# Kernel optimization log

Hardware: AMD Instinct MI355X
Metric: run time of the kernel (lower is better)

Reference implementation:

```python
import jax, jax.numpy as jnp
import numpy as np

B, S, D, H = 2, 2048, 1024, 16
DK = D // H


def setup_inputs() -> dict:
    key = jax.random.key(0)
    ks = jax.random.split(key, 8)
    s = 1.0 / np.sqrt(D)
    return {
        "query": jax.random.normal(ks[0], (B, S, D), jnp.float32),
        "key": jax.random.normal(ks[1], (B, S, D), jnp.float32),
        "value": jax.random.normal(ks[2], (B, S, D), jnp.float32),
        "mask": jnp.ones((B, S), jnp.int32),
        "w_q": jax.random.normal(ks[3], (D, D), jnp.float32) * s,
        "w_k": jax.random.normal(ks[4], (D, D), jnp.float32) * s,
        "w_v": jax.random.normal(ks[5], (D, D), jnp.float32) * s,
        "w_o": jax.random.normal(ks[6], (D, D), jnp.float32) * s,
        "b_o": jnp.zeros((D,), jnp.float32),
    }


def reference(query, key, value, mask, w_q, w_k, w_v, w_o, b_o):
    scale = np.sqrt(DK).astype(np.float32)
    # Linear layers: torch stores weight as [out, in], y = x @ W.T
    Q = (query @ w_q.T).reshape(B, S, H, DK).transpose(0, 2, 1, 3)  # [B,H,S,DK]
    K = (key @ w_k.T).reshape(B, S, H, DK).transpose(0, 2, 1, 3)
    V = (value @ w_v.T).reshape(B, S, H, DK).transpose(0, 2, 1, 3)
    scores = jnp.einsum("bhqd,bhkd->bhqk", Q, K) / scale  # [B,H,S,S]
    m = mask[:, None, None, :]  # [B,1,1,S]
    scores = jnp.where(m == 0, jnp.float32(-1e9), scores)
    attn = jax.nn.softmax(scores, axis=-1)  # dropout in eval mode = identity
    ctx = jnp.einsum("bhqk,bhkd->bhqd", attn, V)
    ctx = ctx.transpose(0, 2, 1, 3).reshape(B, S, D)
    out = ctx @ w_o.T + b_o
    return out, attn
```

## Files before the change

### kernel.cpp

```cpp
#include <hip/hip_runtime.h>
#include <hip/hip_bf16.h>
#include <math.h>

#define B 2
#define S 2048
#define D 1024
#define H 16
#define DK 64

typedef __attribute__((ext_vector_type(8))) short bf8;
typedef __attribute__((ext_vector_type(8))) unsigned short u16x8;
typedef __attribute__((ext_vector_type(4))) unsigned short u16x4;
typedef __attribute__((ext_vector_type(4))) float f32x4;
typedef unsigned short ush;

__device__ __forceinline__ float bf2f(ush u) {
    union { unsigned int i; float f; } v; v.i = ((unsigned int)u) << 16; return v.f;
}
__device__ __forceinline__ ush f2bf_rne(float x) {
    __hip_bfloat16 h = __float2bfloat16(x);
    union { __hip_bfloat16 h; ush u; } v; v.h = h; return v.u;
}
__device__ __forceinline__ ush f2bf_trunc(float x) {
    union { float f; unsigned int i; } v; v.f = x; return (ush)(v.i >> 16);
}

__device__ __forceinline__ void gl16(const void* g, void* l) {
    __builtin_amdgcn_global_load_lds(
        (const __attribute__((address_space(1))) void*)g,
        (__attribute__((address_space(3))) void*)l, 16, 0, 0);
}

#define FENCE()    asm volatile("" ::: "memory")
#define WAIT_VM(N) asm volatile("s_waitcnt vmcnt(" #N ")" ::: "memory")
#define BARRAW()   __builtin_amdgcn_s_barrier()

__global__ __launch_bounds__(256) void conv_tri_k(
    const float* __restrict__ A, ush* __restrict__ Ah, ush* __restrict__ Al, int nbA,
    const float* __restrict__ Bsrc, ush* __restrict__ Bh, ush* __restrict__ Bl, int nbB,
    const float* __restrict__ C, ush* __restrict__ Ch)
{
    const int bx = blockIdx.x;
    const float* src; ush* oh; ush* ol; size_t t;
    if (bx < nbA)            { src = A;    oh = Ah; ol = Al;      t = (size_t)bx * 256 + threadIdx.x; }
    else if (bx < nbA + nbB) { src = Bsrc; oh = Bh; ol = Bl;      t = (size_t)(bx - nbA) * 256 + threadIdx.x; }
    else                     { src = C;    oh = Ch; ol = nullptr; t = (size_t)(bx - nbA - nbB) * 256 + threadIdx.x; }

    const float4* s4 = (const float4*)src + t * 2;
    float4 a = s4[0], c = s4[1];
    float v[8] = {a.x, a.y, a.z, a.w, c.x, c.y, c.z, c.w};
    u16x8 hi;
#pragma unroll
    for (int j = 0; j < 8; ++j) hi[j] = f2bf_trunc(v[j]);
    *(u16x8*)&oh[t * 8] = hi;
    if (ol) {
        u16x8 lo;
#pragma unroll
        for (int j = 0; j < 8; ++j) lo[j] = f2bf_rne(v[j] - bf2f(hi[j]));
        *(u16x8*)&ol[t * 8] = lo;
    }
}

template<bool SPLIT, int EPI>
__global__ __launch_bounds__(512) void gemm_bf3(
    const ush* __restrict__ Xh, const ush* __restrict__ Xl,
    const ush* __restrict__ Wh, const ush* __restrict__ Wl,
    const float* __restrict__ bias, void* __restrict__ Y0v, void* __restrict__ Y1v)
{
    const int tid  = threadIdx.x;
    const int lane = tid & 63;
    const int w    = tid >> 6;
    const int wn   = w >> 2;
    const int wm   = w & 3;
    const int m0   = blockIdx.x * 128;
    const int n0   = blockIdx.y * 128;

    __shared__ __align__(16) ush BufS[4][256 * 64];

    f32x4 acc[4][2];
#pragma unroll
    for (int s = 0; s < 4; ++s)
#pragma unroll
        for (int t = 0; t < 2; ++t) acc[s][t] = (f32x4){0.f, 0.f, 0.f, 0.f};

    const int kg = (lane >> 4) * 8;
    const int rb = lane >> 3;
    const int jd = lane & 7;
    const int kS = SPLIT ? 32 : 16;

    auto stage = [&](ush* buf, int ks) {
#pragma unroll
        for (int i = 0; i < 4; ++i) {
            int rd = w * 32 + i * 8 + rb;
            int jo = jd ^ (rd & 7);
            const ush* src;
            if (rd < 128) {
                if (SPLIT)
                    src = (jo < 4) ? Xh + (size_t)(n0 + rd) * 1024 + ks * 32 + jo * 8
                                   : Xl + (size_t)(n0 + rd) * 1024 + ks * 32 + (jo - 4) * 8;
                else
                    src = Xh + (size_t)(n0 + rd) * 1024 + ks * 64 + jo * 8;
            } else {
                int rw = rd - 128;
                if (SPLIT)
                    src = (jo < 4) ? Wh + (size_t)(m0 + rw) * 1024 + ks * 32 + jo * 8
                                   : Wl + (size_t)(m0 + rw) * 1024 + ks * 32 + (jo - 4) * 8;
                else
                    src = Wh + (size_t)(m0 + rw) * 1024 + ks * 64 + jo * 8;
            }
            gl16(src, &buf[(w * 32 + i * 8) * 64]);
        }
    };

    auto step = [&](const ush* buf) {
        bf8 a0[4], a1[4], b0[2], b1[2];
#pragma unroll
        for (int s = 0; s < 4; ++s) {
            int r = wn * 64 + s * 16 + (lane & 15);
            a0[s] = *(const bf8*)&buf[r * 64 + (kg ^ ((r & 7) << 3))];
            a1[s] = *(const bf8*)&buf[r * 64 + ((32 + kg) ^ ((r & 7) << 3))];
        }
#pragma unroll
        for (int t = 0; t < 2; ++t) {
            int r = wm * 32 + t * 16 + (lane & 15);
            b0[t] = *(const bf8*)&buf[(128 + r) * 64 + (kg ^ ((r & 7) << 3))];
            b1[t] = *(const bf8*)&buf[(128 + r) * 64 + ((32 + kg) ^ ((r & 7) << 3))];
        }
#pragma unroll
        for (int s = 0; s < 4; ++s)
#pragma unroll
            for (int t = 0; t < 2; ++t) {
                acc[s][t] = __builtin_amdgcn_mfma_f32_16x16x32_bf16(a0[s], b0[t], acc[s][t], 0, 0, 0);
                if (SPLIT) {
                    acc[s][t] = __builtin_amdgcn_mfma_f32_16x16x32_bf16(a0[s], b1[t], acc[s][t], 0, 0, 0);
                    acc[s][t] = __builtin_amdgcn_mfma_f32_16x16x32_bf16(a1[s], b0[t], acc[s][t], 0, 0, 0);
                } else {
                    acc[s][t] = __builtin_amdgcn_mfma_f32_16x16x32_bf16(a1[s], b1[t], acc[s][t], 0, 0, 0);
                }
            }
    };

    stage(&BufS[0][0], 0);
    stage(&BufS[1][0], 1);
    stage(&BufS[2][0], 2);
    FENCE();
    WAIT_VM(8); BARRAW(); FENCE();

    for (int kt = 0; kt < kS; ++kt) {
        const int pf = kt + 3;
        if (pf < kS) { stage(&BufS[pf & 3][0], pf); FENCE(); }
        step(&BufS[kt & 3][0]);
        if (kt + 3 < kS)      { WAIT_VM(8); }
        else if (kt + 2 < kS) { WAIT_VM(4); }
        else if (kt + 1 < kS) { WAIT_VM(0); }
        BARRAW(); FENCE();
    }

#pragma unroll
    for (int s = 0; s < 4; ++s)
#pragma unroll
        for (int t = 0; t < 2; ++t) {
            const int nb = n0 + wn * 64 + 16 * s + 4 * (lane >> 4);
            const int m  = m0 + wm * 32 + 16 * t + (lane & 15);
            if (EPI == 0) {
                float* Y = (float*)Y0v;
                const float bb = bias[m];
#pragma unroll
                for (int r = 0; r < 4; ++r)
                    Y[(size_t)(nb + r) * 1024 + m] = acc[s][t][r] + bb;
            } else if (EPI == 1) {
                ush* Yh = (ush*)Y0v;
                ush* Yl = (ush*)Y1v;
#pragma unroll
                for (int r = 0; r < 4; ++r) {
                    float v = acc[s][t][r];
                    ush hi = f2bf_trunc(v);
                    Yh[(size_t)(nb + r) * 1024 + m] = hi;
                    Yl[(size_t)(nb + r) * 1024 + m] = f2bf_rne(v - bf2f(hi));
                }
            } else {
                ush* Vt = (ush*)Y0v;
                u16x4 pk;
#pragma unroll
                for (int r = 0; r < 4; ++r) pk[r] = f2bf_rne(acc[s][t][r]);
                size_t addr = ((size_t)(nb >> 11) * 1024 + m) * 2048 + (nb & 2047);
                *(u16x4*)&Vt[addr] = pk;
            }
        }
}

__global__ __launch_bounds__(512) void attn_mfma4(
    const ush* __restrict__ Qh, const ush* __restrict__ Ql,
    const ush* __restrict__ Kh, const ush* __restrict__ Kl,
    const ush* __restrict__ Vt, const int* __restrict__ maskg,
    float* __restrict__ attn, ush* __restrict__ ctx)
{
    const int tid  = threadIdx.x;
    const int lane = tid & 63;
    const int w    = tid >> 6;
    const int lid  = blockIdx.x + (blockIdx.y << 4) + (blockIdx.z << 8);
    const int swz  = ((lid & 7) << 6) | (lid >> 3);
    const int qt = swz & 15, h = (swz >> 4) & 15, b = swz >> 8;
    const int q0 = qt * 128;

    __shared__ __align__(16) ush KhsD[3][4096];
    __shared__ __align__(16) ush KlsD[2][4096];
    __shared__ __align__(16) ush VtsD[2][4096];
    __shared__ __align__(16) ush Pus[8][1024];
    __shared__ float biasS[2048];

    const int kg = (lane >> 4) * 8;
    const int q  = lane & 15;
    const int qrow = q0 + w * 16 + q;
    const int rb = lane >> 3;
    const int jd = lane & 7;

    const ush* KhT = Kh + (size_t)(b * S) * 1024 + h * DK;
    const ush* KlT = Kl + (size_t)(b * S) * 1024 + h * DK;
    const ush* VtT = Vt + (size_t)(b * 1024 + h * DK) * 2048;

    {
        const int t4 = tid * 4;
        int4 mv = *(const int4*)&maskg[b * S + t4];
        biasS[t4 + 0] = mv.x ? 0.f : -1e9f;
        biasS[t4 + 1] = mv.y ? 0.f : -1e9f;
        biasS[t4 + 2] = mv.z ? 0.f : -1e9f;
        biasS[t4 + 3] = mv.w ? 0.f : -1e9f;
    }

    bf8 qh[2], ql[2];
    {
        const ush* p1 = Qh + (size_t)(b * S + qrow) * D + h * DK + kg;
        qh[0] = *(const bf8*)p1; qh[1] = *(const bf8*)(p1 + 32);
        const ush* p2 = Ql + (size_t)(b * S + qrow) * D + h * DK + kg;
        ql[0] = *(const bf8*)p2; ql[1] = *(const bf8*)(p2 + 32);
    }

    const int rd = w * 8 + rb;
    const int jo = jd ^ (rd & 7);

    auto stKh = [&](int bufi, int k0) {
        gl16(KhT + (size_t)(k0 + rd) * 1024 + jo * 8, &KhsD[bufi][(w * 8) * 64]);
    };
    auto stKl = [&](int bufi, int k0) {
        gl16(KlT + (size_t)(k0 + rd) * 1024 + jo * 8, &KlsD[bufi][(w * 8) * 64]);
    };
    auto stVt = [&](int bufi, int k0) {
        gl16(VtT + (size_t)rd * 2048 + k0 + jo * 8, &VtsD[bufi][(w * 8) * 64]);
    };

    const float scale = 0.125f;
    float mrow = -1e30f, lrow = 0.f;

    auto computeA = [&](const ush* Khs_, int k0) {
        f32x4 sacc[4];
#pragma unroll
        for (int st = 0; st < 4; ++st) sacc[st] = (f32x4){0.f, 0.f, 0.f, 0.f};
#pragma unroll
        for (int st = 0; st < 4; ++st) {
            int r = st * 16 + q;
#pragma unroll
            for (int dh = 0; dh < 2; ++dh) {
                bf8 kf = *(const bf8*)&Khs_[r * 64 + ((dh * 32 + kg) ^ ((r & 7) << 3))];
                sacc[st] = __builtin_amdgcn_mfma_f32_16x16x32_bf16(kf, qh[dh], sacc[st], 0, 0, 0);
            }
        }
        f32x4 bias_r[4];
#pragma unroll
        for (int st = 0; st < 4; ++st)
            bias_r[st] = *(const f32x4*)&biasS[k0 + st * 16 + (lane >> 4) * 4];
        float tmax = -1e30f;
#pragma unroll
        for (int st = 0; st < 4; ++st)
#pragma unroll
            for (int rr = 0; rr < 4; ++rr)
                tmax = fmaxf(tmax, sacc[st][rr] * scale + bias_r[st][rr]);
        tmax = fmaxf(tmax, __shfl_xor(tmax, 16));
        tmax = fmaxf(tmax, __shfl_xor(tmax, 32));
        const float nm = fmaxf(mrow, tmax);
        float ts = 0.f;
#pragma unroll
        for (int st = 0; st < 4; ++st)
#pragma unroll
            for (int rr = 0; rr < 4; ++rr)
                ts += __expf(sacc[st][rr] * scale + bias_r[st][rr] - nm);
        ts += __shfl_xor(ts, 16);
        ts += __shfl_xor(ts, 32);
        lrow = lrow * __expf(mrow - nm) + ts;
        mrow = nm;
    };

    stKh(0, 0); stKh(1, 64);
    __syncthreads();
    {
        int cur = 0, nxt = 2;
        for (int kt = 0; kt < 32; ++kt) {
            if (kt + 2 < 32) stKh(nxt, (kt + 2) * 64);
            FENCE();
            computeA(&KhsD[cur][0], kt * 64);
            if (kt < 30) { WAIT_VM(1); } else { WAIT_VM(0); }
            BARRAW(); FENCE();
            cur = (cur == 2) ? 0 : cur + 1;
            nxt = (nxt == 2) ? 0 : nxt + 1;
        }
    }
    const float inv_l = 1.f / lrow;

    f32x4 cacc[4];
#pragma unroll
    for (int dt = 0; dt < 4; ++dt) cacc[dt] = (f32x4){0.f, 0.f, 0.f, 0.f};
    float* attn_bh = attn + (size_t)(b * H + h) * S * S;

    auto computeB = [&](int bsel, int k0) {
        const ush* Khs_ = &KhsD[bsel][0];
        const ush* Kls_ = &KlsD[bsel][0];
        const ush* Vts_ = &VtsD[bsel][0];
        f32x4 sacc[4];
#pragma unroll
        for (int st = 0; st < 4; ++st) sacc[st] = (f32x4){0.f, 0.f, 0.f, 0.f};
#pragma unroll
        for (int st = 0; st < 4; ++st) {
            int r = st * 16 + q;
#pragma unroll
            for (int dh = 0; dh < 2; ++dh) {
                bf8 kf = *(const bf8*)&Khs_[r * 64 + ((dh * 32 + kg) ^ ((r & 7) << 3))];
                bf8 lf = *(const bf8*)&Kls_[r * 64 + ((dh * 32 + kg) ^ ((r & 7) << 3))];
                sacc[st] = __builtin_amdgcn_mfma_f32_16x16x32_bf16(kf, qh[dh], sacc[st], 0, 0, 0);
                sacc[st] = __builtin_amdgcn_mfma_f32_16x16x32_bf16(kf, ql[dh], sacc[st], 0, 0, 0);
                sacc[st] = __builtin_amdgcn_mfma_f32_16x16x32_bf16(lf, qh[dh], sacc[st], 0, 0, 0);
            }
        }
#pragma unroll
        for (int st = 0; st < 4; ++st) {
            f32x4 bias_r = *(const f32x4*)&biasS[k0 + st * 16 + (lane >> 4) * 4];
            float pv[4];
#pragma unroll
            for (int rr = 0; rr < 4; ++rr)
                pv[rr] = __expf(sacc[st][rr] * scale + bias_r[rr] - mrow) * inv_l;
            float4 f4 = {pv[0], pv[1], pv[2], pv[3]};
            *(float4*)&attn_bh[(size_t)(q0 + w * 16 + q) * S + k0 + st * 16 + (lane >> 4) * 4] = f4;
#pragma unroll
            for (int rp = 0; rp < 2; ++rp) {
                int key = st * 16 + (lane >> 4) * 4 + rp * 2;
                unsigned int pk = (unsigned int)f2bf_rne(pv[rp * 2]) |
                                  ((unsigned int)f2bf_rne(pv[rp * 2 + 1]) << 16);
                *(unsigned int*)&Pus[w][q * 64 + (key ^ ((q & 7) << 3))] = pk;
            }
        }
        bf8 pa[2];
        pa[0] = *(const bf8*)&Pus[w][q * 64 + ((kg)      ^ ((q & 7) << 3))];
        pa[1] = *(const bf8*)&Pus[w][q * 64 + ((32 + kg) ^ ((q & 7) << 3))];
#pragma unroll
        for (int dt = 0; dt < 4; ++dt) {
            int r = dt * 16 + q;
#pragma unroll
            for (int kc2 = 0; kc2 < 2; ++kc2) {
                bf8 vf = *(const bf8*)&Vts_[r * 64 + ((kc2 * 32 + kg) ^ ((r & 7) << 3))];
                cacc[dt] = __builtin_amdgcn_mfma_f32_16x16x32_bf16(pa[kc2], vf, cacc[dt], 0, 0, 0);
            }
        }
    };

    stKh(0, 0); stKl(0, 0); stVt(0, 0);
    FENCE();
    WAIT_VM(0); BARRAW(); FENCE();
    {
        int cur = 0;
        for (int kt = 0; kt < 32; ++kt) {
            if (kt + 1 < 32) {
                const int kN = (kt + 1) * 64;
                stKh(cur ^ 1, kN); stKl(cur ^ 1, kN); stVt(cur ^ 1, kN);
            }
            FENCE();
            computeB(cur, kt * 64);
            if (kt + 1 < 32) { WAIT_VM(4); } else { FENCE(); }
            BARRAW(); FENCE();
            cur ^= 1;
        }
    }

#pragma unroll
    for (int dt = 0; dt < 4; ++dt)
#pragma unroll
        for (int rr = 0; rr < 4; ++rr) {
            int qq = q0 + w * 16 + 4 * (lane >> 4) + rr;
            ctx[(size_t)(b * S + qq) * D + h * DK + dt * 16 + (lane & 15)] =
                f2bf_rne(cacc[dt][rr]);
        }
}

extern "C" void kernel_launch(void* const* d_in, const int* in_sizes, int n_in,
                              void* d_out, int out_size, void* d_ws, size_t ws_size,
                              hipStream_t stream)
{
    const float* query = (const float*)d_in[0];
    const float* key   = (const float*)d_in[1];
    const float* value = (const float*)d_in[2];
    const int*   mask  = (const int*)d_in[3];
    const float* w_q   = (const float*)d_in[4];
    const float* w_k   = (const float*)d_in[5];
    const float* w_v   = (const float*)d_in[6];
    const float* w_o   = (const float*)d_in[7];
    const float* b_o   = (const float*)d_in[8];

    float* out  = (float*)d_out;
    float* attn = out + (size_t)B * S * D;

    const size_t NE = (size_t)B * S * D;
    const size_t WE = (size_t)D * D;

    ush* Qh = (ush*)d_ws;
    ush* Ql = Qh + NE;
    ush* Kh = Ql + NE;
    ush* Kl = Kh + NE;
    ush* Vt = Kl + NE;
    ush* Cb = Vt + NE;

    ush* qXh = (ush*)attn;
    ush* qXl = qXh + NE;
    ush* kXh = qXl + NE;
    ush* kXl = kXh + NE;
    ush* vXh = kXl + NE;
    ush* wqH = vXh + NE;
    ush* wqL = wqH + WE;
    ush* wkH = wqL + WE;
    ush* wkL = wkH + WE;
    ush* wvH = wkL + WE;
    ush* woH = Qh;

    const dim3 blk(256);
    const dim3 gblk(512);
    const dim3 ggrid(D / 128, (B * S) / 128);
    const dim3 agrid(S / 128, H, B);

    const int nbX = (int)(NE / 8 / 256);
    const int nbW = (int)(WE / 8 / 256);

    conv_tri_k<<<dim3(nbX + nbW + nbX), blk, 0, stream>>>(
        query, qXh, qXl, nbX, w_q, wqH, wqL, nbW, value, vXh);
    conv_tri_k<<<dim3(nbX + nbW + nbW), blk, 0, stream>>>(
        key, kXh, kXl, nbX, w_k, wkH, wkL, nbW, w_v, wvH);

    gemm_bf3<true, 1><<<ggrid, gblk, 0, stream>>>(qXh, qXl, wqH, wqL, nullptr, Qh, Ql);
    gemm_bf3<true, 1><<<ggrid, gblk, 0, stream>>>(kXh, kXl, wkH, wkL, nullptr, Kh, Kl);
    gemm_bf3<false, 2><<<ggrid, gblk, 0, stream>>>(vXh, nullptr, wvH, nullptr, nullptr, Vt, nullptr);

    attn_mfma4<<<agrid, dim3(512), 0, stream>>>(Qh, Ql, Kh, Kl, Vt, mask, attn, Cb);

    conv_tri_k<<<dim3(nbW), blk, 0, stream>>>(
        nullptr, nullptr, nullptr, 0, nullptr, nullptr, nullptr, 0, w_o, woH);
    gemm_bf3<false, 0><<<ggrid, gblk, 0, stream>>>(Cb, nullptr, woH, nullptr, b_o, out, nullptr);
}
```

Baseline: 344.4 us.

## Merge conversion and QKV projection launches; use nontemporal stores for outputs

Folds the two input-conversion launches into one kernel that dispatches on block index, and folds the three Q/K/V projection GEMMs into one launch that picks the projection from blockIdx.z. The aim is fewer kernel launches and less tail idle time, since a single larger grid can fill the GPU while the three GEMMs run together. The attention-probability stores and the output GEMM stores now use nontemporal stores to avoid polluting the cache with large write-only data. The risk is heterogeneous work inside the merged GEMM grid (the V path does half the MFMA steps), which gives uneven block durations.

```diff
diff --git a/kernel.cpp b/kernel.cpp
--- a/kernel.cpp
+++ b/kernel.cpp
@@ -35,37 +35,64 @@
 #define WAIT_VM(N) asm volatile("s_waitcnt vmcnt(" #N ")" ::: "memory")
 #define BARRAW()   __builtin_amdgcn_s_barrier()
 
-__global__ __launch_bounds__(256) void conv_tri_k(
-    const float* __restrict__ A, ush* __restrict__ Ah, ush* __restrict__ Al, int nbA,
-    const float* __restrict__ Bsrc, ush* __restrict__ Bh, ush* __restrict__ Bl, int nbB,
-    const float* __restrict__ C, ush* __restrict__ Ch)
-{
-    const int bx = blockIdx.x;
-    const float* src; ush* oh; ush* ol; size_t t;
-    if (bx < nbA)            { src = A;    oh = Ah; ol = Al;      t = (size_t)bx * 256 + threadIdx.x; }
-    else if (bx < nbA + nbB) { src = Bsrc; oh = Bh; ol = Bl;      t = (size_t)(bx - nbA) * 256 + threadIdx.x; }
-    else                     { src = C;    oh = Ch; ol = nullptr; t = (size_t)(bx - nbA - nbB) * 256 + threadIdx.x; }
+__global__ __launch_bounds__(256) void conv_hex_k(
+    const float* __restrict__ q,  ush* __restrict__ qh,  ush* __restrict__ qlo,
+    const float* __restrict__ wq, ush* __restrict__ wqh, ush* __restrict__ wql,
+    const float* __restrict__ k,  ush* __restrict__ kh,  ush* __restrict__ klo,
+    const float* __restrict__ wk, ush* __restrict__ wkh, ush* __restrict__ wkl,
+    const float* __restrict__ v,  ush* __restrict__ vh,
+    const float* __restrict__ wv, ush* __restrict__ wvh,
+    int nbX, int nbW)
+{
+    int bx = blockIdx.x;
+    const float* src; ush* oh; ush* ol;
+    if (bx < nbX) { src = q; oh = qh; ol = qlo; }
+    else { bx -= nbX;
+      if (bx < nbW) { src = wq; oh = wqh; ol = wql; }
+      else { bx -= nbW;
+        if (bx < nbX) { src = k; oh = kh; ol = klo; }
+        else { bx -= nbX;
+          if (bx < nbW) { src = wk; oh = wkh; ol = wkl; }
+          else { bx -= nbW;
+            if (bx < nbX) { src = v; oh = vh; ol = nullptr; }
+            else { bx -= nbX; src = wv; oh = wvh; ol = nullptr; }
+          } } } }
+    const size_t t = (size_t)bx * 256 + threadIdx.x;
 
     const float4* s4 = (const float4*)src + t * 2;
+    float4 a = s4[0], c = s4[1];
+    float vv[8] = {a.x, a.y, a.z, a.w, c.x, c.y, c.z, c.w};
+    u16x8 hi;
+#pragma unroll
+    for (int j = 0; j < 8; ++j) hi[j] = f2bf_trunc(vv[j]);
+    *(u16x8*)&oh[t * 8] = hi;
+    if (ol) {
+        u16x8 lo;
+#pragma unroll
+        for (int j = 0; j < 8; ++j) lo[j] = f2bf_rne(vv[j] - bf2f(hi[j]));
+        *(u16x8*)&ol[t * 8] = lo;
+    }
+}
+
+__global__ __launch_bounds__(256) void conv_hi_k(
+    const float* __restrict__ X, ush* __restrict__ Oh)
+{
+    const size_t t = (size_t)blockIdx.x * 256 + threadIdx.x;
+    const float4* s4 = (const float4*)X + t * 2;
     float4 a = s4[0], c = s4[1];
     float v[8] = {a.x, a.y, a.z, a.w, c.x, c.y, c.z, c.w};
     u16x8 hi;
 #pragma unroll
     for (int j = 0; j < 8; ++j) hi[j] = f2bf_trunc(v[j]);
-    *(u16x8*)&oh[t * 8] = hi;
-    if (ol) {
-        u16x8 lo;
-#pragma unroll
-        for (int j = 0; j < 8; ++j) lo[j] = f2bf_rne(v[j] - bf2f(hi[j]));
-        *(u16x8*)&ol[t * 8] = lo;
-    }
+    *(u16x8*)&Oh[t * 8] = hi;
 }
 
 template<bool SPLIT, int EPI>
-__global__ __launch_bounds__(512) void gemm_bf3(
+__device__ __forceinline__ void gemm_body(
     const ush* __restrict__ Xh, const ush* __restrict__ Xl,
     const ush* __restrict__ Wh, const ush* __restrict__ Wl,
-    const float* __restrict__ bias, void* __restrict__ Y0v, void* __restrict__ Y1v)
+    const float* __restrict__ bias, void* __restrict__ Y0v, void* __restrict__ Y1v,
+    ush* BufS)
 {
     const int tid  = threadIdx.x;
     const int lane = tid & 63;
@@ -74,8 +101,6 @@
     const int wm   = w & 3;
     const int m0   = blockIdx.x * 128;
     const int n0   = blockIdx.y * 128;
-
-    __shared__ __align__(16) ush BufS[4][256 * 64];
 
     f32x4 acc[4][2];
 #pragma unroll
@@ -140,16 +165,16 @@
             }
     };
 
-    stage(&BufS[0][0], 0);
-    stage(&BufS[1][0], 1);
-    stage(&BufS[2][0], 2);
+    stage(&BufS[0 * 16384], 0);
+    stage(&BufS[1 * 16384], 1);
+    stage(&BufS[2 * 16384], 2);
     FENCE();
     WAIT_VM(8); BARRAW(); FENCE();
 
     for (int kt = 0; kt < kS; ++kt) {
         const int pf = kt + 3;
-        if (pf < kS) { stage(&BufS[pf & 3][0], pf); FENCE(); }
-        step(&BufS[kt & 3][0]);
+        if (pf < kS) { stage(&BufS[(pf & 3) * 16384], pf); FENCE(); }
+        step(&BufS[(kt & 3) * 16384]);
         if (kt + 3 < kS)      { WAIT_VM(8); }
         else if (kt + 2 < kS) { WAIT_VM(4); }
         else if (kt + 1 < kS) { WAIT_VM(0); }
@@ -167,7 +192,8 @@
                 const float bb = bias[m];
 #pragma unroll
                 for (int r = 0; r < 4; ++r)
-                    Y[(size_t)(nb + r) * 1024 + m] = acc[s][t][r] + bb;
+                    __builtin_nontemporal_store(acc[s][t][r] + bb,
+                                                &Y[(size_t)(nb + r) * 1024 + m]);
             } else if (EPI == 1) {
                 ush* Yh = (ush*)Y0v;
                 ush* Yl = (ush*)Y1v;
@@ -187,6 +213,31 @@
                 *(u16x4*)&Vt[addr] = pk;
             }
         }
+}
+
+__global__ __launch_bounds__(512) void gemm_proj3(
+    const ush* __restrict__ qXh, const ush* __restrict__ qXl,
+    const ush* __restrict__ wqH, const ush* __restrict__ wqL,
+    ush* __restrict__ Qh, ush* __restrict__ Ql,
+    const ush* __restrict__ kXh, const ush* __restrict__ kXl,
+    const ush* __restrict__ wkH, const ush* __restrict__ wkL,
+    ush* __restrict__ Kh, ush* __restrict__ Kl,
+    const ush* __restrict__ vXh, const ush* __restrict__ wvH,
+    ush* __restrict__ Vt)
+{
+    __shared__ __align__(16) ush BufS[4 * 256 * 64];
+    const int z = blockIdx.z;
+    if (z == 0)      gemm_body<true, 1>(qXh, qXl, wqH, wqL, nullptr, Qh, Ql, BufS);
+    else if (z == 1) gemm_body<true, 1>(kXh, kXl, wkH, wkL, nullptr, Kh, Kl, BufS);
+    else             gemm_body<false, 2>(vXh, nullptr, wvH, nullptr, nullptr, Vt, nullptr, BufS);
+}
+
+__global__ __launch_bounds__(512) void gemm_outk(
+    const ush* __restrict__ Xh, const ush* __restrict__ Wh,
+    const float* __restrict__ bias, float* __restrict__ Y)
+{
+    __shared__ __align__(16) ush BufS[4 * 256 * 64];
+    gemm_body<false, 0>(Xh, nullptr, Wh, nullptr, bias, Y, nullptr, BufS);
 }
 
 __global__ __launch_bounds__(512) void attn_mfma4(
@@ -333,17 +384,17 @@
 #pragma unroll
         for (int st = 0; st < 4; ++st) {
             f32x4 bias_r = *(const f32x4*)&biasS[k0 + st * 16 + (lane >> 4) * 4];
-            float pv[4];
+            f32x4 pvv;
 #pragma unroll
             for (int rr = 0; rr < 4; ++rr)
-                pv[rr] = __expf(sacc[st][rr] * scale + bias_r[rr] - mrow) * inv_l;
-            float4 f4 = {pv[0], pv[1], pv[2], pv[3]};
-            *(float4*)&attn_bh[(size_t)(q0 + w * 16 + q) * S + k0 + st * 16 + (lane >> 4) * 4] = f4;
+                pvv[rr] = __expf(sacc[st][rr] * scale + bias_r[rr] - mrow) * inv_l;
+            __builtin_nontemporal_store(pvv,
+                (f32x4*)&attn_bh[(size_t)(q0 + w * 16 + q) * S + k0 + st * 16 + (lane >> 4) * 4]);
 #pragma unroll
             for (int rp = 0; rp < 2; ++rp) {
                 int key = st * 16 + (lane >> 4) * 4 + rp * 2;
-                unsigned int pk = (unsigned int)f2bf_rne(pv[rp * 2]) |
-                                  ((unsigned int)f2bf_rne(pv[rp * 2 + 1]) << 16);
+                unsigned int pk = (unsigned int)f2bf_rne(pvv[rp * 2]) |
+                                  ((unsigned int)f2bf_rne(pvv[rp * 2 + 1]) << 16);
                 *(unsigned int*)&Pus[w][q * 64 + (key ^ ((q & 7) << 3))] = pk;
             }
         }
@@ -430,24 +481,25 @@
 
     const dim3 blk(256);
     const dim3 gblk(512);
-    const dim3 ggrid(D / 128, (B * S) / 128);
+    const dim3 pgrid(D / 128, (B * S) / 128, 3);
+    const dim3 ogrid(D / 128, (B * S) / 128);
     const dim3 agrid(S / 128, H, B);
 
     const int nbX = (int)(NE / 8 / 256);
     const int nbW = (int)(WE / 8 / 256);
 
-    conv_tri_k<<<dim3(nbX + nbW + nbX), blk, 0, stream>>>(
-        query, qXh, qXl, nbX, w_q, wqH, wqL, nbW, value, vXh);
-    conv_tri_k<<<dim3(nbX + nbW + nbW), blk, 0, stream>>>(
-        key, kXh, kXl, nbX, w_k, wkH, wkL, nbW, w_v, wvH);
-
-    gemm_bf3<true, 1><<<ggrid, gblk, 0, stream>>>(qXh, qXl, wqH, wqL, nullptr, Qh, Ql);
-    gemm_bf3<true, 1><<<ggrid, gblk, 0, stream>>>(kXh, kXl, wkH, wkL, nullptr, Kh, Kl);
-    gemm_bf3<false, 2><<<ggrid, gblk, 0, stream>>>(vXh, nullptr, wvH, nullptr, nullptr, Vt, nullptr);
-
-    attn_mfma4<<<agrid, dim3(512), 0, stream>>>(Qh, Ql, Kh, Kl, Vt, mask, attn, Cb);
-
-    conv_tri_k<<<dim3(nbW), blk, 0, stream>>>(
-        nullptr, nullptr, nullptr, 0, nullptr, nullptr, nullptr, 0, w_o, woH);
-    gemm_bf3<false, 0><<<ggrid, gblk, 0, stream>>>(Cb, nullptr, woH, nullptr, b_o, out, nullptr);
-}
+    conv_hex_k<<<dim3(3 * nbX + 3 * nbW), blk, 0, stream>>>(
+        query, qXh, qXl, w_q, wqH, wqL,
+        key,   kXh, kXl, w_k, wkH, wkL,
+        value, vXh, w_v, wvH, nbX, nbW);
+
+    gemm_proj3<<<pgrid, gblk, 0, stream>>>(
+        qXh, qXl, wqH, wqL, Qh, Ql,
+        kXh, kXl, wkH, wkL, Kh, Kl,
+        vXh, wvH, Vt);
+
+    attn_mfma4<<<agrid, gblk, 0, stream>>>(Qh, Ql, Kh, Kl, Vt, mask, attn, Cb);
+
+    conv_hi_k<<<dim3(nbW), blk, 0, stream>>>(w_o, woH);
+    gemm_outk<<<ogrid, gblk, 0, stream>>>(Cb, woH, b_o, out);
+}
```

Result: faster. 319.4 us (-7.2%).
